# Kernel optimization log

Hardware: AMD Instinct MI355X
Metric: run time of the kernel (lower is better)

The kernel has to match this reference:

```python
import jax, jax.numpy as jnp
import numpy as np

B, C, H, W = 8, 512, 32, 32
NUM_HEADS, D_K = 8, 64
EPS = 1e-5


def setup_inputs() -> dict:
    key = jax.random.key(0)
    ks = jax.random.split(key, 6)
    s = 1.0 / np.sqrt(C)
    return {
        "x": jax.random.normal(ks[0], (B, C, H, W), dtype=jnp.float32),
        "wq": jax.random.uniform(ks[1], (C, NUM_HEADS * D_K), jnp.float32, -s, s),
        "bq": jnp.zeros((NUM_HEADS * D_K,), jnp.float32),
        "wk": jax.random.uniform(ks[2], (C, NUM_HEADS * D_K), jnp.float32, -s, s),
        "bk": jnp.zeros((NUM_HEADS * D_K,), jnp.float32),
        "wv": jax.random.uniform(ks[3], (C, NUM_HEADS * D_K), jnp.float32, -s, s),
        "bv": jnp.zeros((NUM_HEADS * D_K,), jnp.float32),
        "ln_g": jnp.ones((C,), jnp.float32),
        "ln_b": jnp.zeros((C,), jnp.float32),
        "wo": jax.random.uniform(ks[4], (NUM_HEADS * D_K, C), jnp.float32, -s, s),
        "bo": jnp.zeros((C,), jnp.float32),
    }


def reference(x, wq, bq, wk, bk, wv, bv, ln_g, ln_b, wo, bo):
    b, c, h, w = x.shape
    seq = h * w
    # [B, C, H, W] -> [B, S, C]
    t = x.reshape(b, c, seq).transpose(0, 2, 1)
    residual = t
    # LayerNorm over channel dim
    mu = jnp.mean(t, axis=-1, keepdims=True)
    var = jnp.var(t, axis=-1, keepdims=True)
    tn = (t - mu) * jax.lax.rsqrt(var + EPS) * ln_g + ln_b
    # QKV projections -> [B, S, h, d]
    q = (tn @ wq + bq).reshape(b, seq, NUM_HEADS, D_K)
    k = (tn @ wk + bk).reshape(b, seq, NUM_HEADS, D_K)
    v = (tn @ wv + bv).reshape(b, seq, NUM_HEADS, D_K)
    scores = jnp.einsum("bqhd,bkhd->bhqk", q, k) / np.sqrt(D_K).astype(np.float32)
    attn = jax.nn.softmax(scores, axis=-1)
    out = jnp.einsum("bhqk,bkhd->bqhd", attn, v).reshape(b, seq, NUM_HEADS * D_K)
    out = out @ wo + bo
    return out + residual
```

## Files before the change

kernel.cpp:

```cpp
#include <hip/hip_runtime.h>
#include <hip/hip_bf16.h>
#include <stdint.h>

#define BB 8
#define CC 512
#define SS 1024
#define NH 8
#define DK 64
#define MM (BB*SS)
#define PQ 72

typedef __attribute__((ext_vector_type(8))) short bf16x8;
typedef __attribute__((ext_vector_type(4))) float f32x4;

__device__ inline float b2f(unsigned short u) {
    union { unsigned int i; float f; } x; x.i = ((unsigned int)u) << 16; return x.f;
}
__device__ inline unsigned short f2b(float f) {
    union { float f; unsigned int i; } x; x.f = f;
    unsigned int r = (x.i + 0x7FFFu + ((x.i >> 16) & 1u)) >> 16;
    return (unsigned short)r;
}
__device__ inline unsigned int cvtpk(float lo, float hi) {
    unsigned int r;
    asm("v_cvt_pk_bf16_f32 %0, %1, %2" : "=v"(r) : "v"(lo), "v"(hi));
    return r;
}
__device__ inline f32x4 mfma16(bf16x8 a, bf16x8 b, f32x4 c) {
    return __builtin_amdgcn_mfma_f32_16x16x32_bf16(a, b, c, 0, 0, 0);
}
__device__ __forceinline__ void gload16(const void* g, void* l) {
    __builtin_amdgcn_global_load_lds(
        (const __attribute__((address_space(1))) void*)g,
        (__attribute__((address_space(3))) void*)l, 16, 0, 0);
}

__global__ void wtrans_kernel(const float* __restrict__ wq, const float* __restrict__ wk,
                              const float* __restrict__ wv, const float* __restrict__ wo,
                              unsigned short* __restrict__ wT) {
    __shared__ float lds[32][33];
    const float* w = (blockIdx.z == 0) ? wq : (blockIdx.z == 1) ? wk : (blockIdx.z == 2) ? wv : wo;
    unsigned short* o = wT + (size_t)blockIdx.z * (512 * 512);
    const int n0 = blockIdx.x * 32, k0 = blockIdx.y * 32;
    const int tx = threadIdx.x, ty = threadIdx.y;
#pragma unroll
    for (int i = 0; i < 4; ++i)
        lds[ty + 8 * i][tx] = w[(size_t)(k0 + ty + 8 * i) * 512 + n0 + tx];
    __syncthreads();
#pragma unroll
    for (int i = 0; i < 4; ++i)
        o[(size_t)(n0 + ty + 8 * i) * 512 + k0 + tx] = f2b(lds[tx][ty + 8 * i]);
}

__global__ void xtrans_kernel(const float* __restrict__ x, unsigned short* __restrict__ xt) {
    __shared__ float lds[32][33];
    const int s0 = blockIdx.x * 32, c0 = blockIdx.y * 32, b = blockIdx.z;
    const int tx = threadIdx.x, ty = threadIdx.y;
#pragma unroll
    for (int i = 0; i < 4; ++i)
        lds[ty + 8 * i][tx] = x[((size_t)b * 512 + c0 + ty + 8 * i) * 1024 + s0 + tx];
    __syncthreads();
#pragma unroll
    for (int i = 0; i < 4; ++i)
        xt[((size_t)b * 1024 + s0 + ty + 8 * i) * 512 + c0 + tx] = f2b(lds[tx][ty + 8 * i]);
}

__global__ void __launch_bounds__(256) ln_kernel(const unsigned short* __restrict__ xt,
                                                 const float* __restrict__ g,
                                                 const float* __restrict__ bta,
                                                 unsigned short* __restrict__ tn) {
    const int t = threadIdx.x, lane = t & 63, w = t >> 6;
    const int row = blockIdx.x * 4 + w;
    bf16x8 v = *(const bf16x8*)(xt + (size_t)row * 512 + lane * 8);
    float f[8], sum = 0.f, sq = 0.f;
#pragma unroll
    for (int e = 0; e < 8; ++e) { f[e] = b2f((unsigned short)v[e]); sum += f[e]; sq += f[e] * f[e]; }
#pragma unroll
    for (int m = 1; m <= 32; m <<= 1) { sum += __shfl_xor(sum, m); sq += __shfl_xor(sq, m); }
    const float mean = sum * (1.f / 512.f);
    const float var = sq * (1.f / 512.f) - mean * mean;
    const float rstd = rsqrtf(var + 1e-5f);
    const float4 g0 = *(const float4*)(g + lane * 8), g1 = *(const float4*)(g + lane * 8 + 4);
    const float4 b0 = *(const float4*)(bta + lane * 8), b1 = *(const float4*)(bta + lane * 8 + 4);
    const float gg[8] = {g0.x, g0.y, g0.z, g0.w, g1.x, g1.y, g1.z, g1.w};
    const float bb[8] = {b0.x, b0.y, b0.z, b0.w, b1.x, b1.y, b1.z, b1.w};
    bf16x8 out;
#pragma unroll
    for (int e = 0; e < 8; ++e)
        out[e] = (short)f2b((f[e] - mean) * rstd * gg[e] + bb[e]);
    *(bf16x8*)(tn + (size_t)row * 512 + lane * 8) = out;
}

__device__ inline void gemm_tile(const unsigned short* __restrict__ A,
                                 const unsigned short* __restrict__ Bt,
                                 int m0, int n0,
                                 unsigned short* A_lds, unsigned short* B_lds,
                                 f32x4 acc[4][4]) {
    const int t = threadIdx.x;
    const int lane = t & 63, w = t >> 6;
    const int l15 = lane & 15, l4 = lane >> 4;
    const int wm = (w >> 1) * 64, wn = (w & 1) * 64;
#pragma unroll 1
    for (int kt = 0; kt < 8; ++kt) {
        __syncthreads();
#pragma unroll
        for (int i = 0; i < 4; ++i) {
            int chunk = i * 256 + t;
            int row = chunk >> 3, kc = (chunk & 7) * 8;
            gload16(A + (size_t)(m0 + row) * 512 + kt * 64 + kc, &A_lds[chunk * 8]);
            gload16(Bt + (size_t)(n0 + row) * 512 + kt * 64 + kc, &B_lds[chunk * 8]);
        }
        __syncthreads();
#pragma unroll
        for (int kk = 0; kk < 2; ++kk) {
            bf16x8 af[4], bfr[4];
#pragma unroll
            for (int i = 0; i < 4; ++i)
                af[i] = *(const bf16x8*)&A_lds[(wm + i * 16 + l15) * 64 + kk * 32 + l4 * 8];
#pragma unroll
            for (int j = 0; j < 4; ++j)
                bfr[j] = *(const bf16x8*)&B_lds[(wn + j * 16 + l15) * 64 + kk * 32 + l4 * 8];
#pragma unroll
            for (int i = 0; i < 4; ++i)
#pragma unroll
                for (int j = 0; j < 4; ++j)
                    acc[i][j] = mfma16(af[i], bfr[j], acc[i][j]);
        }
    }
}

__global__ void __launch_bounds__(256) gemm_qkv_kernel(const unsigned short* __restrict__ tn,
                                                       const unsigned short* __restrict__ wT,
                                                       const float* __restrict__ bq,
                                                       const float* __restrict__ bk,
                                                       const float* __restrict__ bv,
                                                       unsigned short* __restrict__ outbase) {
    __shared__ alignas(16) unsigned short A_lds[128 * 64];
    __shared__ alignas(16) unsigned short B_lds[128 * 64];
    const int z = blockIdx.z;
    const unsigned short* Bt = wT + (size_t)z * (512 * 512);
    const float* bias = (z == 0) ? bq : (z == 1) ? bk : bv;
    const int m0 = blockIdx.x * 128, n0 = blockIdx.y * 128;
    f32x4 acc[4][4];
    const f32x4 z4 = {0.f, 0.f, 0.f, 0.f};
#pragma unroll
    for (int i = 0; i < 4; ++i)
#pragma unroll
        for (int j = 0; j < 4; ++j) acc[i][j] = z4;
    gemm_tile(tn, Bt, m0, n0, A_lds, B_lds, acc);
    const int lane = threadIdx.x & 63, w = threadIdx.x >> 6;
    const int l15 = lane & 15, l4 = lane >> 4;
    const int wm = (w >> 1) * 64, wn = (w & 1) * 64;
    if (z < 2) {
        unsigned short* out = outbase + (size_t)z * MM * 512;
#pragma unroll
        for (int i = 0; i < 4; ++i)
#pragma unroll
            for (int j = 0; j < 4; ++j) {
                int col = n0 + wn + j * 16 + l15;
                float bcol = bias[col];
#pragma unroll
                for (int r = 0; r < 4; ++r) {
                    int row = m0 + wm + i * 16 + l4 * 4 + r;
                    out[(size_t)row * 512 + col] = f2b(acc[i][j][r] + bcol);
                }
            }
    } else {
        unsigned short* vt = outbase + (size_t)2 * MM * 512;
#pragma unroll
        for (int i = 0; i < 4; ++i)
#pragma unroll
            for (int j = 0; j < 4; ++j) {
                int col = n0 + wn + j * 16 + l15;
                float bcol = bias[col];
                int rowb = m0 + wm + i * 16 + l4 * 4;
                int bi = rowb >> 10, s0 = rowb & 1023;
                unsigned int lo = (unsigned int)f2b(acc[i][j][0] + bcol) |
                                  ((unsigned int)f2b(acc[i][j][1] + bcol) << 16);
                unsigned int hi = (unsigned int)f2b(acc[i][j][2] + bcol) |
                                  ((unsigned int)f2b(acc[i][j][3] + bcol) << 16);
                uint2 pk; pk.x = lo; pk.y = hi;
                *(uint2*)&vt[((size_t)bi * 512 + col) * 1024 + s0] = pk;
            }
    }
}

__global__ void __launch_bounds__(256) attn_kernel(const unsigned short* __restrict__ q,
                                                   const unsigned short* __restrict__ k,
                                                   const unsigned short* __restrict__ vt,
                                                   unsigned short* __restrict__ o) {
    __shared__ alignas(16) unsigned short Kl[2][64 * 64];
    __shared__ alignas(16) unsigned short Vl[2][64 * 64];
    __shared__ alignas(16) unsigned short Pl[4][16 * PQ];
    const int qt = blockIdx.x, h = blockIdx.y, b = blockIdx.z;
    const int t = threadIdx.x, lane = t & 63, w = t >> 6;
    const int l15 = lane & 15, l4 = lane >> 4;

    const int qrow = qt * 64 + w * 16 + l15;
    const unsigned short* qp = q + ((size_t)(b * SS + qrow)) * 512 + h * 64;
    bf16x8 qf[2];
#pragma unroll
    for (int kk = 0; kk < 2; ++kk) {
        bf16x8 tmp = *(const bf16x8*)(qp + kk * 32 + l4 * 8);
#pragma unroll
        for (int e = 0; e < 8; ++e)
            tmp[e] = (short)f2b(b2f((unsigned short)tmp[e]) * 0.125f);
        qf[kk] = tmp;
    }

    const unsigned short* krow_base = k + ((size_t)(b * SS)) * 512 + h * 64;
    const unsigned short* vrow_base = vt + ((size_t)(b * NH + h) * DK) * SS;

    auto STAGE = [&](int bi, int kt) {
        const int key0 = kt * 64;
#pragma unroll
        for (int i = 0; i < 2; ++i) {
            int chunk = i * 256 + t;
            int row = chunk >> 3;
            int scb = ((chunk & 7) * 16) ^ ((row & 7) << 4);
            gload16((const char*)(krow_base + (size_t)(key0 + row) * 512) + scb,
                    &Kl[bi][chunk * 8]);
            gload16((const char*)(vrow_base + (size_t)row * SS + key0) + scb,
                    &Vl[bi][chunk * 8]);
        }
    };

    float m_run = -1e30f, l_run = 0.f;
    f32x4 acc_o[4];
    const f32x4 z4 = {0.f, 0.f, 0.f, 0.f};
#pragma unroll
    for (int j = 0; j < 4; ++j) acc_o[j] = z4;

    STAGE(0, 0);
    __syncthreads();

#pragma unroll 1
    for (int kt = 0; kt < 16; ++kt) {
        const int bi = kt & 1;
        if (kt < 15) STAGE(bi ^ 1, kt + 1);

        f32x4 sc[4];
#pragma unroll
        for (int j = 0; j < 4; ++j) sc[j] = z4;
#pragma unroll
        for (int kk = 0; kk < 2; ++kk)
#pragma unroll
            for (int j = 0; j < 4; ++j) {
                int row = j * 16 + l15;
                int cb = (kk * 64 + l4 * 16) ^ ((row & 7) << 4);
                bf16x8 kf = *(const bf16x8*)((const char*)Kl[bi] + row * 128 + cb);
                sc[j] = mfma16(kf, qf[kk], sc[j]);
            }

        float mx = fmaxf(fmaxf(sc[0][0], sc[0][1]), fmaxf(sc[0][2], sc[0][3]));
#pragma unroll
        for (int j = 1; j < 4; ++j)
            mx = fmaxf(mx, fmaxf(fmaxf(sc[j][0], sc[j][1]), fmaxf(sc[j][2], sc[j][3])));
        mx = fmaxf(mx, __shfl_xor(mx, 16));
        mx = fmaxf(mx, __shfl_xor(mx, 32));
        const float mnew = fmaxf(m_run, mx);
        const float scl = __expf(m_run - mnew);
        m_run = mnew;

        float p[4][4], lsum = 0.f;
#pragma unroll
        for (int j = 0; j < 4; ++j)
#pragma unroll
            for (int r = 0; r < 4; ++r) {
                p[j][r] = __expf(sc[j][r] - mnew);
                lsum += p[j][r];
            }
        l_run = l_run * scl + lsum;

#pragma unroll
        for (int j = 0; j < 4; ++j) {
            uint2 pk;
            pk.x = cvtpk(p[j][0], p[j][1]);
            pk.y = cvtpk(p[j][2], p[j][3]);
            *(uint2*)&Pl[w][l15 * PQ + j * 16 + l4 * 4] = pk;
        }

        float scl_r[4];
#pragma unroll
        for (int r = 0; r < 4; ++r) scl_r[r] = __shfl(scl, (l4 << 2) | r);
#pragma unroll
        for (int j = 0; j < 4; ++j)
#pragma unroll
            for (int r = 0; r < 4; ++r) acc_o[j][r] *= scl_r[r];

#pragma unroll
        for (int kk = 0; kk < 2; ++kk) {
            bf16x8 pf = *(const bf16x8*)&Pl[w][l15 * PQ + kk * 32 + l4 * 8];
#pragma unroll
            for (int j = 0; j < 4; ++j) {
                int row = j * 16 + l15;
                int cb = (kk * 64 + l4 * 16) ^ ((row & 7) << 4);
                bf16x8 vf = *(const bf16x8*)((const char*)Vl[bi] + row * 128 + cb);
                acc_o[j] = mfma16(pf, vf, acc_o[j]);
            }
        }

        __syncthreads();
    }

    float l_tot = l_run;
    l_tot += __shfl_xor(l_tot, 16);
    l_tot += __shfl_xor(l_tot, 32);
    float l_r[4];
#pragma unroll
    for (int r = 0; r < 4; ++r) l_r[r] = __shfl(l_tot, (l4 << 2) | r);

#pragma unroll
    for (int j = 0; j < 4; ++j)
#pragma unroll
        for (int r = 0; r < 4; ++r) {
            int row = qt * 64 + w * 16 + l4 * 4 + r;
            float val = acc_o[j][r] / l_r[r];
            o[((size_t)(b * SS + row)) * 512 + h * 64 + j * 16 + l15] = f2b(val);
        }
}

__global__ void __launch_bounds__(256) gemm_out_kernel(const unsigned short* __restrict__ ao,
                                                       const unsigned short* __restrict__ woT,
                                                       const float* __restrict__ bo,
                                                       const unsigned short* __restrict__ xt,
                                                       float* __restrict__ out) {
    __shared__ alignas(16) unsigned short A_lds[128 * 64];
    __shared__ alignas(16) unsigned short B_lds[128 * 64];
    const int m0 = blockIdx.x * 128, n0 = blockIdx.y * 128;
    f32x4 acc[4][4];
    const f32x4 z4 = {0.f, 0.f, 0.f, 0.f};
#pragma unroll
    for (int i = 0; i < 4; ++i)
#pragma unroll
        for (int j = 0; j < 4; ++j) acc[i][j] = z4;
    gemm_tile(ao, woT, m0, n0, A_lds, B_lds, acc);
    const int lane = threadIdx.x & 63, w = threadIdx.x >> 6;
    const int l15 = lane & 15, l4 = lane >> 4;
    const int wm = (w >> 1) * 64, wn = (w & 1) * 64;
#pragma unroll
    for (int i = 0; i < 4; ++i)
#pragma unroll
        for (int j = 0; j < 4; ++j) {
            int col = n0 + wn + j * 16 + l15;
            float bcol = bo[col];
#pragma unroll
            for (int r = 0; r < 4; ++r) {
                int row = m0 + wm + i * 16 + l4 * 4 + r;
                float resid = b2f(xt[(size_t)row * 512 + col]);
                out[(size_t)row * 512 + col] = acc[i][j][r] + bcol + resid;
            }
        }
}

extern "C" void kernel_launch(void* const* d_in, const int* in_sizes, int n_in,
                              void* d_out, int out_size, void* d_ws, size_t ws_size,
                              hipStream_t stream) {
    const float* x   = (const float*)d_in[0];
    const float* wq  = (const float*)d_in[1];
    const float* bq  = (const float*)d_in[2];
    const float* wk  = (const float*)d_in[3];
    const float* bk  = (const float*)d_in[4];
    const float* wv  = (const float*)d_in[5];
    const float* bv  = (const float*)d_in[6];
    const float* lng = (const float*)d_in[7];
    const float* lnb = (const float*)d_in[8];
    const float* wo  = (const float*)d_in[9];
    const float* bo  = (const float*)d_in[10];
    float* out = (float*)d_out;

    unsigned short* ws  = (unsigned short*)d_ws;
    const size_t M1 = (size_t)1024 * 1024;
    unsigned short* tn   = ws;
    unsigned short* qkvb = ws + 4 * M1;
    unsigned short* wT   = ws + 16 * M1;
    unsigned short* xt   = ws + 17 * M1;
    unsigned short* ao   = tn;

    wtrans_kernel<<<dim3(16, 16, 4), dim3(32, 8), 0, stream>>>(wq, wk, wv, wo, wT);
    xtrans_kernel<<<dim3(32, 16, 8), dim3(32, 8), 0, stream>>>(x, xt);
    ln_kernel<<<2048, 256, 0, stream>>>(xt, lng, lnb, tn);
    gemm_qkv_kernel<<<dim3(64, 4, 3), 256, 0, stream>>>(tn, wT, bq, bk, bv, qkvb);
    attn_kernel<<<dim3(16, 8, 8), 256, 0, stream>>>(qkvb,
                                                    qkvb + (size_t)MM * 512,
                                                    qkvb + (size_t)2 * MM * 512,
                                                    ao);
    gemm_out_kernel<<<dim3(64, 4), 256, 0, stream>>>(ao, wT + (size_t)3 * 512 * 512, bo, xt, out);
}
```

Measured before the change: 188.0 us.

## Fuse LayerNorm with transpose, double-buffer GEMM loads, lazy softmax rescale in attention

Replaces the transpose-then-LN pair with a column stats pass plus a fused transpose/normalize kernel that reads fp32 x directly. The weight transpose now uses 64x64 tiles with vector loads and stores. The GEMM tile loop double-buffers LDS so the next K slice loads while MFMAs run, at the cost of twice the LDS per block. Attention folds log2(e) into the Q scale, uses exp2, and skips the running-max rescale when the max grows by at most 8. It also raises wave priority around the MFMA sections. Stats live in the qkv buffer before the QKV GEMM overwrites it.

```diff
diff --git a/kernel.cpp b/kernel.cpp
--- a/kernel.cpp
+++ b/kernel.cpp
@@ -35,97 +35,146 @@
         (__attribute__((address_space(3))) void*)l, 16, 0, 0);
 }
 
-__global__ void wtrans_kernel(const float* __restrict__ wq, const float* __restrict__ wk,
-                              const float* __restrict__ wv, const float* __restrict__ wo,
-                              unsigned short* __restrict__ wT) {
-    __shared__ float lds[32][33];
+__global__ void __launch_bounds__(256) wtrans_kernel(const float* __restrict__ wq,
+                                                     const float* __restrict__ wk,
+                                                     const float* __restrict__ wv,
+                                                     const float* __restrict__ wo,
+                                                     unsigned short* __restrict__ wT) {
+    __shared__ float lds[64][65];
     const float* w = (blockIdx.z == 0) ? wq : (blockIdx.z == 1) ? wk : (blockIdx.z == 2) ? wv : wo;
     unsigned short* o = wT + (size_t)blockIdx.z * (512 * 512);
-    const int n0 = blockIdx.x * 32, k0 = blockIdx.y * 32;
-    const int tx = threadIdx.x, ty = threadIdx.y;
-#pragma unroll
-    for (int i = 0; i < 4; ++i)
-        lds[ty + 8 * i][tx] = w[(size_t)(k0 + ty + 8 * i) * 512 + n0 + tx];
+    const int n0 = blockIdx.x * 64, k0 = blockIdx.y * 64;
+    const int t = threadIdx.x;
+    {
+        const int nl = (t & 15) * 4, kr = t >> 4;
+#pragma unroll
+        for (int i = 0; i < 4; ++i) {
+            float4 v = *(const float4*)(w + (size_t)(k0 + kr + i * 16) * 512 + n0 + nl);
+            lds[kr + i * 16][nl] = v.x; lds[kr + i * 16][nl + 1] = v.y;
+            lds[kr + i * 16][nl + 2] = v.z; lds[kr + i * 16][nl + 3] = v.w;
+        }
+    }
     __syncthreads();
-#pragma unroll
-    for (int i = 0; i < 4; ++i)
-        o[(size_t)(n0 + ty + 8 * i) * 512 + k0 + tx] = f2b(lds[tx][ty + 8 * i]);
-}
-
-__global__ void xtrans_kernel(const float* __restrict__ x, unsigned short* __restrict__ xt) {
-    __shared__ float lds[32][33];
-    const int s0 = blockIdx.x * 32, c0 = blockIdx.y * 32, b = blockIdx.z;
-    const int tx = threadIdx.x, ty = threadIdx.y;
-#pragma unroll
-    for (int i = 0; i < 4; ++i)
-        lds[ty + 8 * i][tx] = x[((size_t)b * 512 + c0 + ty + 8 * i) * 1024 + s0 + tx];
+    {
+        const int k8 = (t & 7) * 8, nr = t >> 3;
+#pragma unroll
+        for (int ii = 0; ii < 2; ++ii) {
+            int n = nr + ii * 32;
+            unsigned short pk[8];
+#pragma unroll
+            for (int e = 0; e < 8; ++e) pk[e] = f2b(lds[k8 + e][n]);
+            *(uint4*)&o[(size_t)(n0 + n) * 512 + k0 + k8] = *(uint4*)pk;
+        }
+    }
+}
+
+__global__ void __launch_bounds__(256) stats_kernel(const float* __restrict__ x,
+                                                    float2* __restrict__ stats) {
+    __shared__ float2 red[16][17];
+    const int b = blockIdx.y, s0 = blockIdx.x * 16;
+    const int sl = threadIdx.x & 15, cg = threadIdx.x >> 4;
+    const float* xp = x + ((size_t)b * 512 + cg * 32) * 1024 + s0 + sl;
+    float sum = 0.f, sq = 0.f;
+#pragma unroll 8
+    for (int i = 0; i < 32; ++i) { float v = xp[(size_t)i * 1024]; sum += v; sq += v * v; }
+    red[cg][sl] = make_float2(sum, sq);
     __syncthreads();
-#pragma unroll
-    for (int i = 0; i < 4; ++i)
-        xt[((size_t)b * 1024 + s0 + ty + 8 * i) * 512 + c0 + tx] = f2b(lds[tx][ty + 8 * i]);
-}
-
-__global__ void __launch_bounds__(256) ln_kernel(const unsigned short* __restrict__ xt,
-                                                 const float* __restrict__ g,
-                                                 const float* __restrict__ bta,
-                                                 unsigned short* __restrict__ tn) {
-    const int t = threadIdx.x, lane = t & 63, w = t >> 6;
-    const int row = blockIdx.x * 4 + w;
-    bf16x8 v = *(const bf16x8*)(xt + (size_t)row * 512 + lane * 8);
-    float f[8], sum = 0.f, sq = 0.f;
-#pragma unroll
-    for (int e = 0; e < 8; ++e) { f[e] = b2f((unsigned short)v[e]); sum += f[e]; sq += f[e] * f[e]; }
-#pragma unroll
-    for (int m = 1; m <= 32; m <<= 1) { sum += __shfl_xor(sum, m); sq += __shfl_xor(sq, m); }
-    const float mean = sum * (1.f / 512.f);
-    const float var = sq * (1.f / 512.f) - mean * mean;
-    const float rstd = rsqrtf(var + 1e-5f);
-    const float4 g0 = *(const float4*)(g + lane * 8), g1 = *(const float4*)(g + lane * 8 + 4);
-    const float4 b0 = *(const float4*)(bta + lane * 8), b1 = *(const float4*)(bta + lane * 8 + 4);
-    const float gg[8] = {g0.x, g0.y, g0.z, g0.w, g1.x, g1.y, g1.z, g1.w};
-    const float bb[8] = {b0.x, b0.y, b0.z, b0.w, b1.x, b1.y, b1.z, b1.w};
-    bf16x8 out;
-#pragma unroll
-    for (int e = 0; e < 8; ++e)
-        out[e] = (short)f2b((f[e] - mean) * rstd * gg[e] + bb[e]);
-    *(bf16x8*)(tn + (size_t)row * 512 + lane * 8) = out;
+    if (threadIdx.x < 16) {
+        float s = 0.f, q = 0.f;
+#pragma unroll
+        for (int c = 0; c < 16; ++c) { s += red[c][threadIdx.x].x; q += red[c][threadIdx.x].y; }
+        float mean = s * (1.f / 512.f);
+        float var = q * (1.f / 512.f) - mean * mean;
+        stats[b * 1024 + s0 + threadIdx.x] = make_float2(mean, rsqrtf(var + 1e-5f));
+    }
+}
+
+__global__ void __launch_bounds__(256) xln_kernel(const float* __restrict__ x,
+                                                  const float2* __restrict__ stats,
+                                                  const float* __restrict__ g,
+                                                  const float* __restrict__ bta,
+                                                  unsigned short* __restrict__ xt,
+                                                  unsigned short* __restrict__ tn) {
+    __shared__ float lds[64][65];
+    const int s0 = blockIdx.x * 64, c0 = blockIdx.y * 64, b = blockIdx.z;
+    const int t = threadIdx.x;
+    {
+        const int sl = (t & 15) * 4, cr = t >> 4;
+#pragma unroll
+        for (int i = 0; i < 4; ++i) {
+            float4 v = *(const float4*)(x + ((size_t)b * 512 + c0 + cr + i * 16) * 1024 + s0 + sl);
+            lds[cr + i * 16][sl] = v.x; lds[cr + i * 16][sl + 1] = v.y;
+            lds[cr + i * 16][sl + 2] = v.z; lds[cr + i * 16][sl + 3] = v.w;
+        }
+    }
+    __syncthreads();
+    {
+        const int c8 = (t & 7) * 8, sr = t >> 3;
+        float gg[8], bb[8];
+        {
+            float4 g0 = *(const float4*)(g + c0 + c8), g1 = *(const float4*)(g + c0 + c8 + 4);
+            float4 b0 = *(const float4*)(bta + c0 + c8), b1 = *(const float4*)(bta + c0 + c8 + 4);
+            gg[0]=g0.x; gg[1]=g0.y; gg[2]=g0.z; gg[3]=g0.w; gg[4]=g1.x; gg[5]=g1.y; gg[6]=g1.z; gg[7]=g1.w;
+            bb[0]=b0.x; bb[1]=b0.y; bb[2]=b0.z; bb[3]=b0.w; bb[4]=b1.x; bb[5]=b1.y; bb[6]=b1.z; bb[7]=b1.w;
+        }
+#pragma unroll
+        for (int ii = 0; ii < 2; ++ii) {
+            int s = sr + ii * 32;
+            float2 st = stats[b * 1024 + s0 + s];
+            unsigned short rawp[8], nrmp[8];
+#pragma unroll
+            for (int e = 0; e < 8; ++e) {
+                float v = lds[c8 + e][s];
+                rawp[e] = f2b(v);
+                nrmp[e] = f2b((v - st.x) * st.y * gg[e] + bb[e]);
+            }
+            *(uint4*)&xt[((size_t)b * 1024 + s0 + s) * 512 + c0 + c8] = *(uint4*)rawp;
+            *(uint4*)&tn[((size_t)b * 1024 + s0 + s) * 512 + c0 + c8] = *(uint4*)nrmp;
+        }
+    }
 }
 
 __device__ inline void gemm_tile(const unsigned short* __restrict__ A,
                                  const unsigned short* __restrict__ Bt,
                                  int m0, int n0,
-                                 unsigned short* A_lds, unsigned short* B_lds,
+                                 unsigned short (*A_lds)[128 * 64],
+                                 unsigned short (*B_lds)[128 * 64],
                                  f32x4 acc[4][4]) {
     const int t = threadIdx.x;
     const int lane = t & 63, w = t >> 6;
     const int l15 = lane & 15, l4 = lane >> 4;
     const int wm = (w >> 1) * 64, wn = (w & 1) * 64;
-#pragma unroll 1
-    for (int kt = 0; kt < 8; ++kt) {
-        __syncthreads();
+    auto STAGE = [&](int bi, int kt) {
 #pragma unroll
         for (int i = 0; i < 4; ++i) {
             int chunk = i * 256 + t;
             int row = chunk >> 3, kc = (chunk & 7) * 8;
-            gload16(A + (size_t)(m0 + row) * 512 + kt * 64 + kc, &A_lds[chunk * 8]);
-            gload16(Bt + (size_t)(n0 + row) * 512 + kt * 64 + kc, &B_lds[chunk * 8]);
-        }
-        __syncthreads();
+            gload16(A + (size_t)(m0 + row) * 512 + kt * 64 + kc, &A_lds[bi][chunk * 8]);
+            gload16(Bt + (size_t)(n0 + row) * 512 + kt * 64 + kc, &B_lds[bi][chunk * 8]);
+        }
+    };
+    STAGE(0, 0);
+    __syncthreads();
+#pragma unroll 1
+    for (int kt = 0; kt < 8; ++kt) {
+        const int bi = kt & 1;
+        if (kt < 7) STAGE(bi ^ 1, kt + 1);
 #pragma unroll
         for (int kk = 0; kk < 2; ++kk) {
             bf16x8 af[4], bfr[4];
 #pragma unroll
             for (int i = 0; i < 4; ++i)
-                af[i] = *(const bf16x8*)&A_lds[(wm + i * 16 + l15) * 64 + kk * 32 + l4 * 8];
+                af[i] = *(const bf16x8*)&A_lds[bi][(wm + i * 16 + l15) * 64 + kk * 32 + l4 * 8];
 #pragma unroll
             for (int j = 0; j < 4; ++j)
-                bfr[j] = *(const bf16x8*)&B_lds[(wn + j * 16 + l15) * 64 + kk * 32 + l4 * 8];
+                bfr[j] = *(const bf16x8*)&B_lds[bi][(wn + j * 16 + l15) * 64 + kk * 32 + l4 * 8];
 #pragma unroll
             for (int i = 0; i < 4; ++i)
 #pragma unroll
                 for (int j = 0; j < 4; ++j)
                     acc[i][j] = mfma16(af[i], bfr[j], acc[i][j]);
         }
+        __syncthreads();
     }
 }
 
@@ -135,8 +184,8 @@
                                                        const float* __restrict__ bk,
                                                        const float* __restrict__ bv,
                                                        unsigned short* __restrict__ outbase) {
-    __shared__ alignas(16) unsigned short A_lds[128 * 64];
-    __shared__ alignas(16) unsigned short B_lds[128 * 64];
+    __shared__ alignas(16) unsigned short A_lds[2][128 * 64];
+    __shared__ alignas(16) unsigned short B_lds[2][128 * 64];
     const int z = blockIdx.z;
     const unsigned short* Bt = wT + (size_t)z * (512 * 512);
     const float* bias = (z == 0) ? bq : (z == 1) ? bk : bv;
@@ -175,11 +224,11 @@
                 float bcol = bias[col];
                 int rowb = m0 + wm + i * 16 + l4 * 4;
                 int bi = rowb >> 10, s0 = rowb & 1023;
-                unsigned int lo = (unsigned int)f2b(acc[i][j][0] + bcol) |
-                                  ((unsigned int)f2b(acc[i][j][1] + bcol) << 16);
-                unsigned int hi = (unsigned int)f2b(acc[i][j][2] + bcol) |
-                                  ((unsigned int)f2b(acc[i][j][3] + bcol) << 16);
-                uint2 pk; pk.x = lo; pk.y = hi;
+                uint2 pk;
+                pk.x = (unsigned int)f2b(acc[i][j][0] + bcol) |
+                       ((unsigned int)f2b(acc[i][j][1] + bcol) << 16);
+                pk.y = (unsigned int)f2b(acc[i][j][2] + bcol) |
+                       ((unsigned int)f2b(acc[i][j][3] + bcol) << 16);
                 *(uint2*)&vt[((size_t)bi * 512 + col) * 1024 + s0] = pk;
             }
     }
@@ -196,6 +245,7 @@
     const int t = threadIdx.x, lane = t & 63, w = t >> 6;
     const int l15 = lane & 15, l4 = lane >> 4;
 
+    const float QSC = 0.125f * 1.44269504f;
     const int qrow = qt * 64 + w * 16 + l15;
     const unsigned short* qp = q + ((size_t)(b * SS + qrow)) * 512 + h * 64;
     bf16x8 qf[2];
@@ -204,7 +254,7 @@
         bf16x8 tmp = *(const bf16x8*)(qp + kk * 32 + l4 * 8);
 #pragma unroll
         for (int e = 0; e < 8; ++e)
-            tmp[e] = (short)f2b(b2f((unsigned short)tmp[e]) * 0.125f);
+            tmp[e] = (short)f2b(b2f((unsigned short)tmp[e]) * QSC);
         qf[kk] = tmp;
     }
 
@@ -242,6 +292,7 @@
         f32x4 sc[4];
 #pragma unroll
         for (int j = 0; j < 4; ++j) sc[j] = z4;
+        __builtin_amdgcn_s_setprio(1);
 #pragma unroll
         for (int kk = 0; kk < 2; ++kk)
 #pragma unroll
@@ -251,26 +302,38 @@
                 bf16x8 kf = *(const bf16x8*)((const char*)Kl[bi] + row * 128 + cb);
                 sc[j] = mfma16(kf, qf[kk], sc[j]);
             }
+        __builtin_amdgcn_s_setprio(0);
 
         float mx = fmaxf(fmaxf(sc[0][0], sc[0][1]), fmaxf(sc[0][2], sc[0][3]));
 #pragma unroll
         for (int j = 1; j < 4; ++j)
             mx = fmaxf(mx, fmaxf(fmaxf(sc[j][0], sc[j][1]), fmaxf(sc[j][2], sc[j][3])));
-        mx = fmaxf(mx, __shfl_xor(mx, 16));
-        mx = fmaxf(mx, __shfl_xor(mx, 32));
-        const float mnew = fmaxf(m_run, mx);
-        const float scl = __expf(m_run - mnew);
-        m_run = mnew;
+
+        if (!__all(mx - m_run <= 8.f)) {
+            mx = fmaxf(mx, __shfl_xor(mx, 16));
+            mx = fmaxf(mx, __shfl_xor(mx, 32));
+            float mnew = fmaxf(m_run, mx);
+            float scl = exp2f(m_run - mnew);
+            m_run = mnew;
+            l_run *= scl;
+            float scl_r[4];
+#pragma unroll
+            for (int r = 0; r < 4; ++r) scl_r[r] = __shfl(scl, (l4 << 2) | r);
+#pragma unroll
+            for (int j = 0; j < 4; ++j)
+#pragma unroll
+                for (int r = 0; r < 4; ++r) acc_o[j][r] *= scl_r[r];
+        }
 
         float p[4][4], lsum = 0.f;
 #pragma unroll
         for (int j = 0; j < 4; ++j)
 #pragma unroll
             for (int r = 0; r < 4; ++r) {
-                p[j][r] = __expf(sc[j][r] - mnew);
+                p[j][r] = exp2f(sc[j][r] - m_run);
                 lsum += p[j][r];
             }
-        l_run = l_run * scl + lsum;
+        l_run += lsum;
 
 #pragma unroll
         for (int j = 0; j < 4; ++j) {
@@ -280,14 +343,7 @@
             *(uint2*)&Pl[w][l15 * PQ + j * 16 + l4 * 4] = pk;
         }
 
-        float scl_r[4];
-#pragma unroll
-        for (int r = 0; r < 4; ++r) scl_r[r] = __shfl(scl, (l4 << 2) | r);
-#pragma unroll
-        for (int j = 0; j < 4; ++j)
-#pragma unroll
-            for (int r = 0; r < 4; ++r) acc_o[j][r] *= scl_r[r];
-
+        __builtin_amdgcn_s_setprio(1);
 #pragma unroll
         for (int kk = 0; kk < 2; ++kk) {
             bf16x8 pf = *(const bf16x8*)&Pl[w][l15 * PQ + kk * 32 + l4 * 8];
@@ -299,6 +355,7 @@
                 acc_o[j] = mfma16(pf, vf, acc_o[j]);
             }
         }
+        __builtin_amdgcn_s_setprio(0);
 
         __syncthreads();
     }
@@ -325,8 +382,8 @@
                                                        const float* __restrict__ bo,
                                                        const unsigned short* __restrict__ xt,
                                                        float* __restrict__ out) {
-    __shared__ alignas(16) unsigned short A_lds[128 * 64];
-    __shared__ alignas(16) unsigned short B_lds[128 * 64];
+    __shared__ alignas(16) unsigned short A_lds[2][128 * 64];
+    __shared__ alignas(16) unsigned short B_lds[2][128 * 64];
     const int m0 = blockIdx.x * 128, n0 = blockIdx.y * 128;
     f32x4 acc[4][4];
     const f32x4 z4 = {0.f, 0.f, 0.f, 0.f};
@@ -376,10 +433,11 @@
     unsigned short* wT   = ws + 16 * M1;
     unsigned short* xt   = ws + 17 * M1;
     unsigned short* ao   = tn;
-
-    wtrans_kernel<<<dim3(16, 16, 4), dim3(32, 8), 0, stream>>>(wq, wk, wv, wo, wT);
-    xtrans_kernel<<<dim3(32, 16, 8), dim3(32, 8), 0, stream>>>(x, xt);
-    ln_kernel<<<2048, 256, 0, stream>>>(xt, lng, lnb, tn);
+    float2* stats = (float2*)qkvb;
+
+    wtrans_kernel<<<dim3(8, 8, 4), 256, 0, stream>>>(wq, wk, wv, wo, wT);
+    stats_kernel<<<dim3(64, 8), 256, 0, stream>>>(x, stats);
+    xln_kernel<<<dim3(16, 8, 8), 256, 0, stream>>>(x, stats, lng, lnb, xt, tn);
     gemm_qkv_kernel<<<dim3(64, 4, 3), 256, 0, stream>>>(tn, wT, bq, bk, bv, qkvb);
     attn_kernel<<<dim3(16, 8, 8), 256, 0, stream>>>(qkvb,
                                                     qkvb + (size_t)MM * 512,
```

Measured after the change: 188.2 us. About the same (+0.1%).
